# Kernel tuning notes

Hardware: AMD Instinct MI355X
Metric: run time of the kernel (lower is better)

## Reference

```python
import jax, jax.numpy as jnp
import numpy as np
from jax import lax

B, S, C, D, V = 256, 50, 40, 256, 20000
T_DIFF = 1000
BETA_START, BETA_END = 1e-4, 2e-2


def _lstm(x, Wih, Whh, bih, bhh):
    # x: [B,S,D]; single-layer LSTM, batch_first, eval mode (no dropout)
    Bb = x.shape[0]
    H = Whh.shape[1]
    def step(carry, xt):
        h, c = carry
        g = xt @ Wih.T + bih + h @ Whh.T + bhh  # [B,4H]
        i, f, gg, o = jnp.split(g, 4, axis=-1)
        i = jax.nn.sigmoid(i); f = jax.nn.sigmoid(f)
        gg = jnp.tanh(gg); o = jax.nn.sigmoid(o)
        c = f * c + i * gg
        h = o * jnp.tanh(c)
        return (h, c), h
    h0 = jnp.zeros((Bb, H), x.dtype)
    (_, _), hs = lax.scan(step, (h0, h0), x.transpose(1, 0, 2))
    return hs.transpose(1, 0, 2)  # [B,S,H]


def setup_inputs() -> dict:
    key = jax.random.key(0)
    ks = jax.random.split(key, 20)
    sc = 0.05
    inp = {
        'input_seqs': jax.random.randint(ks[0], (B, S, C), 0, V),
        'masks': jnp.zeros((B, S), jnp.int32),
        'lengths': jax.random.randint(ks[1], (B,), 1, S + 1),
        'seq_time_step': jax.random.uniform(ks[2], (B, S), jnp.float32),
        'code_masks': jnp.zeros((B, S, C), jnp.int32),
        'diffusion_time_t': jax.random.randint(ks[3], (B,), 0, T_DIFF),
        'normal_noise': jax.random.normal(ks[4], (B, S, D), jnp.float32),
        # learned parameters
        'emb': jax.random.normal(ks[5], (V + 1, D), jnp.float32) * sc,
        'Wih': jax.random.normal(ks[6], (4 * D, D), jnp.float32) * sc,
        'Whh': jax.random.normal(ks[7], (4 * D, D), jnp.float32) * sc,
        'bih': jnp.zeros((4 * D,), jnp.float32),
        'bhh': jnp.zeros((4 * D,), jnp.float32),
        'Whk': jax.random.normal(ks[8], (D, D), jnp.float32) * sc,
        'bhk': jnp.zeros((D,), jnp.float32),
        'W1': jax.random.normal(ks[9], (64, 2 * D), jnp.float32) * sc,
        'b1': jnp.zeros((64,), jnp.float32),
        'W2': jax.random.normal(ks[10], (2, 64), jnp.float32) * sc,
        'b2': jnp.zeros((2,), jnp.float32),
        'Wdiff': jax.random.normal(ks[11], (D, D), jnp.float32) * sc,
        'bdiff': jnp.zeros((D,), jnp.float32),
        'temb': jax.random.normal(ks[12], (T_DIFF, D), jnp.float32) * sc,
        'Wout': jax.random.normal(ks[13], (2, D), jnp.float32) * sc,
        'bout': jnp.zeros((2,), jnp.float32),
    }
    # padding_idx row zeroed like nn.Embedding(padding_idx=-1)
    inp['emb'] = inp['emb'].at[V].set(0.0)
    return inp


def reference(input_seqs, masks, lengths, seq_time_step, code_masks,
              diffusion_time_t, normal_noise,
              emb, Wih, Whh, bih, bhh, Whk, bhk, W1, b1, W2, b2,
              Wdiff, bdiff, temb, Wout, bout):
    # embedding sum over codes per visit
    x = emb[input_seqs].sum(axis=2)  # [B,S,D]
    rnn_out = _lstm(x, Wih, Whh, bih, bhh)  # [B,S,D]

    # vectorized alignment loop: e_k is ALWAYS x[:,0] (as in source),
    # position i>=1 attends between e_k and w_hk(rnn_out[i-1])
    w = rnn_out @ Whk.T + bhk  # [B,S,D]
    e_k = x[:, :1, :]  # [B,1,D]
    wprev = w[:, :-1, :]  # [B,S-1,D] -> timestep i uses w[i-1]
    cat = jnp.concatenate([jnp.broadcast_to(e_k, wprev.shape), wprev], -1)
    attn = jax.nn.softmax(jnp.tanh(cat @ W1.T + b1) @ W2.T + b2, axis=-1)  # [B,S-1,2]
    aligned_rest = e_k * attn[..., 0:1] + wprev * attn[..., 1:2]
    aligned_e_t = jnp.concatenate([e_k, aligned_rest], axis=1)  # [B,S,D]

    # diffusion noising (linear beta schedule as in ehr.yml defaults)
    betas = jnp.linspace(BETA_START, BETA_END, T_DIFF, dtype=jnp.float32)
    alpha = jnp.cumprod(1.0 - betas)[diffusion_time_t][:, None, None]
    noisy = aligned_e_t * jnp.sqrt(alpha) + normal_noise * jnp.sqrt(1.0 - alpha)

    # UNet surrogate (source unavailable): timestep-conditioned linear map
    predicted_noise = (noisy + temb[diffusion_time_t][:, None, :]) @ Wdiff + bdiff

    gen_x = aligned_e_t + (normal_noise - predicted_noise)
    pool_x = jnp.max(x, axis=1) @ Wout.T + bout  # [B,2]
    gen_pool_x = jnp.max(gen_x, axis=1) @ Wout.T + bout  # [B,2]
    return (pool_x, gen_pool_x, predicted_noise, normal_noise)
```

## Files before the change

### kernel.cpp

```cpp
#include <hip/hip_runtime.h>
#include <cmath>

#define Bb 256
#define Ss 50
#define Cc 40
#define Dd 256
#define Vv 20000

typedef __bf16 bf16;
typedef __bf16 bf16x8 __attribute__((ext_vector_type(8)));
typedef float f32x4 __attribute__((ext_vector_type(4)));
typedef unsigned long long u64;

#define GL2LDS(g, l) __builtin_amdgcn_global_load_lds( \
    (__attribute__((address_space(1))) void*)(g), \
    (__attribute__((address_space(3))) void*)(l), 16, 0, 0)

#define OFFB_GATES    0ull
#define OFFB_ALIGNED  0ull
#define OFFB_CAT      13107200ull
#define OFFB_TMPB     25952256ull
#define OFFB_H1       32505856ull
#define OFFB_ATTNW    35717120ull
#define OFFB_X        52428800ull
#define OFFB_XB       65536000ull
#define OFFB_RNNB     72089600ull
#define OFFB_W        78643200ull
#define OFFB_BAR      91750400ull
#define OFFB_WIHB     92012544ull
#define OFFB_WHHB     92536832ull
#define OFFB_WHKB     93061120ull
#define OFFB_W1B      93192192ull
#define OFFB_WDTB     93257728ull
#define OFFB_SALPHA   93388800ull
#define OFFB_SBETA    93389824ull

template<int BM, int BN, int ACT>
__global__ __launch_bounds__(256) void mfma_gemm(
    const bf16* __restrict__ A, int lda,
    const bf16* __restrict__ B, int ldb,
    const float* __restrict__ bias1, const float* __restrict__ bias2,
    float* __restrict__ C, int ldc, int K)
{
    constexpr int BK = 32;
    constexpr int NF = BN / 32;
    __shared__ bf16 As[BM * BK];
    __shared__ bf16 Bs[BN * BK];
    const int tid  = threadIdx.x;
    const int wave = tid >> 6;
    const int lane = tid & 63;
    const int m0 = blockIdx.x * BM;
    const int n0 = blockIdx.y * BN;
    const int wm = (wave >> 1) * 64;
    const int wn = (wave & 1) * (BN / 2);

    f32x4 acc[4][NF];
#pragma unroll
    for (int i = 0; i < 4; ++i)
#pragma unroll
        for (int j = 0; j < NF; ++j) acc[i][j] = (f32x4){0.f, 0.f, 0.f, 0.f};

    const int ar = tid >> 2;
    const int ac = tid & 3;
    const int sw = ac ^ (ar & 3);
    const int lr = lane & 15;
    const int q  = lane >> 4;

    for (int k0 = 0; k0 < K; k0 += BK) {
        __syncthreads();
#pragma unroll
        for (int it = 0; it < BM / 64; ++it) {
            const bf16* gp = A + (size_t)(m0 + it * 64 + ar) * lda + k0 + sw * 8;
            GL2LDS(gp, As + it * 2048 + wave * 512);
        }
#pragma unroll
        for (int it = 0; it < BN / 64; ++it) {
            const bf16* gp = B + (size_t)(n0 + it * 64 + ar) * ldb + k0 + sw * 8;
            GL2LDS(gp, Bs + it * 2048 + wave * 512);
        }
        __syncthreads();

        bf16x8 af[4], bfv[NF];
#pragma unroll
        for (int fm = 0; fm < 4; ++fm) {
            int m = wm + fm * 16 + lr;
            af[fm] = *(const bf16x8*)(As + m * 32 + ((q ^ (m & 3)) * 8));
        }
#pragma unroll
        for (int fn = 0; fn < NF; ++fn) {
            int n = wn + fn * 16 + lr;
            bfv[fn] = *(const bf16x8*)(Bs + n * 32 + ((q ^ (n & 3)) * 8));
        }
#pragma unroll
        for (int fm = 0; fm < 4; ++fm)
#pragma unroll
            for (int fn = 0; fn < NF; ++fn)
                acc[fm][fn] = __builtin_amdgcn_mfma_f32_16x16x32_bf16(
                    af[fm], bfv[fn], acc[fm][fn], 0, 0, 0);
    }

    const int rbase = q * 4;
#pragma unroll
    for (int fn = 0; fn < NF; ++fn) {
        const int col = n0 + wn + fn * 16 + lr;
        float bb = 0.f;
        if (bias1) bb += bias1[col];
        if (bias2) bb += bias2[col];
#pragma unroll
        for (int fm = 0; fm < 4; ++fm) {
            f32x4 v = acc[fm][fn];
#pragma unroll
            for (int r = 0; r < 4; ++r) {
                const int row = m0 + wm + fm * 16 + rbase + r;
                float val = v[r] + bb;
                if (ACT == 1) val = tanhf(val);
                C[(size_t)row * ldc + col] = val;
            }
        }
    }
}

__global__ __launch_bounds__(512, 2) void lstm_quad(
    const bf16* __restrict__ Whhb,
    const float* __restrict__ gates,
    bf16* __restrict__ rnnb,
    unsigned* __restrict__ bar)
{
    __shared__ bf16 hb0[16 * 256];
    __shared__ bf16 hb1[16 * 256];
    __shared__ float pacc[4][4][16][16];
    const int tid  = threadIdx.x;
    const int w    = tid >> 6;
    const int lane = tid & 63;
    const int lr   = lane & 15;
    const int q    = lane >> 4;
    const int bm   = blockIdx.x & 15;
    const int bd   = blockIdx.x >> 4;
    const int kh   = w >> 2;
    const int ct   = w & 3;
    const int dg   = bd * 64 + ct * 16 + lr;

    f32x4 wfr[4][4];
#pragma unroll
    for (int g = 0; g < 4; ++g) {
        const bf16* brow = Whhb + (size_t)(g * 256 + dg) * Dd + kh * 128 + q * 8;
#pragma unroll
        for (int kc = 0; kc < 4; ++kc)
            wfr[g][kc] = *(const f32x4*)(brow + kc * 32);
    }

    const float* gp[4];
#pragma unroll
    for (int r = 0; r < 4; ++r)
        gp[r] = gates + (size_t)(bm * 16 + q * 4 + r) * (Ss * 1024) + dg;

    const int xrow = tid >> 4, xc8 = tid & 15;
    const size_t my_base = ((size_t)(bm * 16 + xrow) * Ss) * Dd + bd * 64 + xc8 * 4;
    const int pack_off = xrow * 512 + (((bd * 8 + (xc8 >> 1)) ^ (xrow & 7)) << 4) + (xc8 & 1) * 8;

    const int pA  = tid >> 8;
    const int pdA = pA + (pA >= bd ? 1 : 0);
    const int pdB = 2 + (2 >= bd ? 1 : 0);
    const int rowA = (tid >> 4) & 15, xqA = tid & 15;
    const size_t gA = ((size_t)(bm * 16 + rowA) * Ss) * Dd + pdA * 64 + xqA * 4;
    const size_t gB = ((size_t)(bm * 16 + xrow) * Ss) * Dd + pdB * 64 + xc8 * 4;
    const int unpA = rowA * 512 + (((pdA * 8 + (xqA >> 1)) ^ (rowA & 7)) << 4) + (xqA & 1) * 8;
    const int unpB = xrow * 512 + (((pdB * 8 + (xc8 >> 1)) ^ (xrow & 7)) << 4) + (xc8 & 1) * 8;
    unsigned* myf = bar + (bm * 4 + bd) * 32;
    unsigned* pfA = bar + (bm * 4 + pdA) * 32;
    unsigned* pfB = bar + (bm * 4 + pdB) * 32;

    int ew_off[4];
#pragma unroll
    for (int r = 0; r < 4; ++r) {
        const int row = q * 4 + r;
        ew_off[r] = row * 512 + (((dg >> 3) ^ (row & 7)) << 4) + (dg & 7) * 2;
    }

    float c[4] = {0.f, 0.f, 0.f, 0.f};
    float gaA[4][4], gaB[4][4];
    if (kh == 0) {
#pragma unroll
        for (int r = 0; r < 4; ++r)
#pragma unroll
            for (int g = 0; g < 4; ++g) gaA[g][r] = gp[r][g * 256];
    }

#define STEP(T, GACUR, GANEXT, RD, WR, FIRST)                                   \
    {                                                                           \
        f32x4 acc[4];                                                           \
        _Pragma("unroll")                                                       \
        for (int g = 0; g < 4; ++g) acc[g] = (f32x4){0.f, 0.f, 0.f, 0.f};       \
        if (!(FIRST)) {                                                         \
            bf16x8 af[4];                                                       \
            _Pragma("unroll")                                                   \
            for (int kc = 0; kc < 4; ++kc)                                      \
                af[kc] = *(const bf16x8*)((const char*)(RD) + lr * 512          \
                         + (((kh * 16 + kc * 4 + q) ^ (lr & 7)) << 4));         \
            _Pragma("unroll")                                                   \
            for (int kc = 0; kc < 4; ++kc)                                      \
                _Pragma("unroll")                                               \
                for (int g = 0; g < 4; ++g)                                     \
                    acc[g] = __builtin_amdgcn_mfma_f32_16x16x32_bf16(           \
                        af[kc], __builtin_bit_cast(bf16x8, wfr[g][kc]),         \
                        acc[g], 0, 0, 0);                                       \
        }                                                                       \
        if (kh == 1) {                                                          \
            _Pragma("unroll")                                                   \
            for (int g = 0; g < 4; ++g)                                         \
                _Pragma("unroll")                                               \
                for (int r = 0; r < 4; ++r)                                     \
                    pacc[ct][g][q * 4 + r][lr] = acc[g][r];                     \
        }                                                                       \
        __syncthreads();                          \
        if (kh == 0) {                                                          \
            _Pragma("unroll")                                                   \
            for (int r = 0; r < 4; ++r) {                                       \
                float gi = acc[0][r] + pacc[ct][0][q * 4 + r][lr] + GACUR[0][r];\
                float gf = acc[1][r] + pacc[ct][1][q * 4 + r][lr] + GACUR[1][r];\
                float gg = acc[2][r] + pacc[ct][2][q * 4 + r][lr] + GACUR[2][r];\
                float go = acc[3][r] + pacc[ct][3][q * 4 + r][lr] + GACUR[3][r];\
                float ii  = 1.f / (1.f + expf(-gi));                            \
                float ff  = 1.f / (1.f + expf(-gf));                            \
                float g2t = tanhf(gg);                                          \
                float oo  = 1.f / (1.f + expf(-go));                            \
                c[r] = ff * c[r] + ii * g2t;                                    \
                *(bf16*)((char*)(WR) + ew_off[r]) = (bf16)(oo * tanhf(c[r]));   \
            }                                                                   \
        }                                                                       \
        __syncthreads();                          \
        if (tid < 256) {                                                        \
            u64 v = *(const u64*)((const char*)(WR) + pack_off);                \
            __hip_atomic_store((u64*)(rnnb + my_base + (size_t)(T) * Dd), v,    \
                               __ATOMIC_RELAXED, __HIP_MEMORY_SCOPE_AGENT);     \
        }                                                                       \
        if ((T) != Ss - 1) {                                                    \
            __syncthreads();        \
            if (tid == 0)                                                       \
                __hip_atomic_store(myf, (unsigned)((T) + 1),                    \
                                   __ATOMIC_RELAXED, __HIP_MEMORY_SCOPE_AGENT); \
            if (kh == 0) {            \
                _Pragma("unroll")                                               \
                for (int r = 0; r < 4; ++r)                                     \
                    _Pragma("unroll")                                           \
                    for (int g = 0; g < 4; ++g)                                 \
                        GANEXT[g][r] = gp[r][(size_t)((T) + 1) * 1024 + g * 256];\
            }                                                                   \
            while (__hip_atomic_load(pfA, __ATOMIC_RELAXED,                     \
                                     __HIP_MEMORY_SCOPE_AGENT)                  \
                   < (unsigned)((T) + 1)) {}                                    \
            {                                                                   \
                u64 rv = __hip_atomic_load(                                     \
                    (const u64*)(rnnb + gA + (size_t)(T) * Dd),                 \
                    __ATOMIC_RELAXED, __HIP_MEMORY_SCOPE_AGENT);                \
                *(u64*)((char*)(WR) + unpA) = rv;                               \
            }                                                                   \
            if (tid < 256) {                                                    \
                while (__hip_atomic_load(pfB, __ATOMIC_RELAXED,                 \
                                         __HIP_MEMORY_SCOPE_AGENT)              \
                       < (unsigned)((T) + 1)) {}                                \
                u64 rv = __hip_atomic_load(                                     \
                    (const u64*)(rnnb + gB + (size_t)(T) * Dd),                 \
                    __ATOMIC_RELAXED, __HIP_MEMORY_SCOPE_AGENT);                \
                *(u64*)((char*)(WR) + unpB) = rv;                               \
            }                                                                   \
            __syncthreads();           \
        }                                                                       \
    }

    for (int t2 = 0; t2 < Ss; t2 += 2) {
        STEP(t2,     gaA, gaB, hb1, hb0, (t2 == 0));
        STEP(t2 + 1, gaB, gaA, hb0, hb1, false);
    }
#undef STEP
}

__global__ __launch_bounds__(256) void prep_kernel(
    const float* __restrict__ Wih, bf16* __restrict__ Wihb,
    const float* __restrict__ Whh, bf16* __restrict__ Whhb,
    const float* __restrict__ Whk, bf16* __restrict__ Whkb,
    const float* __restrict__ W1,  bf16* __restrict__ W1b,
    const float* __restrict__ Wdiff, bf16* __restrict__ WdTb,
    const int* __restrict__ tdiff, float* __restrict__ salpha,
    float* __restrict__ sbeta, unsigned* __restrict__ bar)
{
    __shared__ float t[32][33];
    int bx = blockIdx.x;
    const int tid = threadIdx.x;
    if (bx < 1024) { int i = bx * 256 + tid; Wihb[i] = (bf16)Wih[i]; return; }
    bx -= 1024;
    if (bx < 1024) { int i = bx * 256 + tid; Whhb[i] = (bf16)Whh[i]; return; }
    bx -= 1024;
    if (bx < 256)  { int i = bx * 256 + tid; Whkb[i] = (bf16)Whk[i]; return; }
    bx -= 256;
    if (bx < 128)  { int i = bx * 256 + tid; W1b[i]  = (bf16)W1[i];  return; }
    bx -= 128;
    if (bx < 64) {
        const int c0 = (bx & 7) * 32, r0 = (bx >> 3) * 32;
        const int tx = tid & 31, ty = tid >> 5;
        for (int i = ty; i < 32; i += 8)
            t[i][tx] = Wdiff[(size_t)(r0 + i) * 256 + c0 + tx];
        __syncthreads();
        for (int i = ty; i < 32; i += 8)
            WdTb[(size_t)(c0 + i) * 256 + r0 + tx] = (bf16)t[tx][i];
        return;
    }
#pragma unroll
    for (int j = 0; j < 8; ++j) bar[tid * 8 + j] = 0u;
    const int tt = tdiff[tid];
    const float step = (0.02f - 1e-4f) / 999.f;
    float prod = 1.f;
    for (int j = 0; j <= tt; ++j) prod *= (1.f - (1e-4f + j * step));
    salpha[tid] = sqrtf(prod);
    sbeta[tid]  = sqrtf(fmaxf(1.f - prod, 0.f));
}

__global__ __launch_bounds__(256) void embed_kernel(
    const int* __restrict__ seqs, const float* __restrict__ emb,
    float* __restrict__ x, bf16* __restrict__ xb)
{
    __shared__ int idx[Cc];
    const int bs = blockIdx.x;
    const int tid = threadIdx.x;
    if (tid < Cc) idx[tid] = seqs[(size_t)bs * Cc + tid];
    __syncthreads();
    float s = 0.f;
#pragma unroll 8
    for (int c = 0; c < Cc; ++c) s += emb[(size_t)idx[c] * Dd + tid];
    x[(size_t)bs * Dd + tid]  = s;
    xb[(size_t)bs * Dd + tid] = (bf16)s;
}

__global__ __launch_bounds__(256) void cat_build_kernel(
    const float* __restrict__ x, const float* __restrict__ w, bf16* __restrict__ cat)
{
    const int r = blockIdx.x;
    const int b = r / (Ss - 1), t = r % (Ss - 1);
    const int d = threadIdx.x;
    cat[(size_t)r * 512 + d]       = (bf16)x[((size_t)b * Ss) * Dd + d];
    cat[(size_t)r * 512 + 256 + d] = (bf16)w[((size_t)b * Ss + t) * Dd + d];
}

__global__ __launch_bounds__(256) void attn2_kernel(
    const float* __restrict__ H1, const float* __restrict__ W2,
    const float* __restrict__ b2, float* __restrict__ attnw)
{
    const int r = blockIdx.x * 4 + (threadIdx.x >> 6);
    const int j = threadIdx.x & 63;
    float h = H1[(size_t)r * 64 + j];
    float v0 = h * W2[j];
    float v1 = h * W2[64 + j];
#pragma unroll
    for (int off = 32; off; off >>= 1) { v0 += __shfl_down(v0, off); v1 += __shfl_down(v1, off); }
    if (j == 0) {
        float z0 = v0 + b2[0], z1 = v1 + b2[1];
        float m = fmaxf(z0, z1);
        float e0 = expf(z0 - m), e1 = expf(z1 - m);
        float inv = 1.f / (e0 + e1);
        attnw[(size_t)r * 2 + 0] = e0 * inv;
        attnw[(size_t)r * 2 + 1] = e1 * inv;
    }
}

__global__ __launch_bounds__(256) void attn_diff_kernel(
    const float* __restrict__ x, const float* __restrict__ w,
    const float* __restrict__ attnw, const float* __restrict__ noise,
    const float* __restrict__ temb, const int* __restrict__ tdiff,
    const float* __restrict__ salpha, const float* __restrict__ sbeta,
    float* __restrict__ aligned, bf16* __restrict__ tmpb)
{
    const int bs = blockIdx.x;
    const int b = bs / Ss, s = bs % Ss;
    const int d = threadIdx.x;
    const float ek = x[((size_t)b * Ss) * Dd + d];
    float v;
    if (s == 0) {
        v = ek;
    } else {
        const int r = b * (Ss - 1) + (s - 1);
        const float a0 = attnw[(size_t)r * 2], a1 = attnw[(size_t)r * 2 + 1];
        v = ek * a0 + w[((size_t)b * Ss + s - 1) * Dd + d] * a1;
    }
    const size_t i = (size_t)bs * Dd + d;
    aligned[i] = v;
    const int t = tdiff[b];
    tmpb[i] = (bf16)(v * salpha[b] + noise[i] * sbeta[b] + temb[(size_t)t * Dd + d]);
}

__device__ inline void pool_reduce_write(float m, const float* __restrict__ Wout,
                                         const float* __restrict__ bout,
                                         float* __restrict__ outp, int b,
                                         float* r0, float* r1)
{
    float v0 = m * Wout[threadIdx.x];
    float v1 = m * Wout[Dd + threadIdx.x];
#pragma unroll
    for (int off = 32; off; off >>= 1) { v0 += __shfl_down(v0, off); v1 += __shfl_down(v1, off); }
    const int lane = threadIdx.x & 63, wv = threadIdx.x >> 6;
    if (lane == 0) { r0[wv] = v0; r1[wv] = v1; }
    __syncthreads();
    if (threadIdx.x == 0) {
        outp[b * 2 + 0] = r0[0] + r0[1] + r0[2] + r0[3] + bout[0];
        outp[b * 2 + 1] = r1[0] + r1[1] + r1[2] + r1[3] + bout[1];
    }
}

__global__ __launch_bounds__(256) void pool_x_kernel(
    const float* __restrict__ x, const float* __restrict__ Wout,
    const float* __restrict__ bout, float* __restrict__ outp)
{
    __shared__ float r0[4], r1[4];
    const int b = blockIdx.x, d = threadIdx.x;
    float m = -INFINITY;
    for (int s = 0; s < Ss; ++s) m = fmaxf(m, x[((size_t)b * Ss + s) * Dd + d]);
    pool_reduce_write(m, Wout, bout, outp, b, r0, r1);
}

__global__ __launch_bounds__(256) void gen_pool_kernel(
    const float* __restrict__ aligned, const float* __restrict__ noise,
    const float* __restrict__ pred, const float* __restrict__ Wout,
    const float* __restrict__ bout, float* __restrict__ outp)
{
    __shared__ float r0[4], r1[4];
    const int b = blockIdx.x, d = threadIdx.x;
    float m = -INFINITY;
    for (int s = 0; s < Ss; ++s) {
        const size_t i = ((size_t)b * Ss + s) * Dd + d;
        m = fmaxf(m, aligned[i] + noise[i] - pred[i]);
    }
    pool_reduce_write(m, Wout, bout, outp, b, r0, r1);
}

extern "C" void kernel_launch(void* const* d_in, const int* in_sizes, int n_in,
                              void* d_out, int out_size, void* d_ws, size_t ws_size,
                              hipStream_t stream)
{
    const int*   seqs  = (const int*)d_in[0];
    const int*   tdiff = (const int*)d_in[5];
    const float* noise = (const float*)d_in[6];
    const float* emb   = (const float*)d_in[7];
    const float* Wih   = (const float*)d_in[8];
    const float* Whh   = (const float*)d_in[9];
    const float* bih   = (const float*)d_in[10];
    const float* bhh   = (const float*)d_in[11];
    const float* Whk   = (const float*)d_in[12];
    const float* bhk   = (const float*)d_in[13];
    const float* W1    = (const float*)d_in[14];
    const float* b1    = (const float*)d_in[15];
    const float* W2    = (const float*)d_in[16];
    const float* b2    = (const float*)d_in[17];
    const float* Wdiff = (const float*)d_in[18];
    const float* bdiff = (const float*)d_in[19];
    const float* temb  = (const float*)d_in[20];
    const float* Wout  = (const float*)d_in[21];
    const float* bout  = (const float*)d_in[22];

    float* outp = (float*)d_out;
    char*  wsb  = (char*)d_ws;

    float* gates   = (float*)(wsb + OFFB_GATES);
    float* aligned = (float*)(wsb + OFFB_ALIGNED);
    bf16*  catb    = (bf16*) (wsb + OFFB_CAT);
    bf16*  tmpb    = (bf16*) (wsb + OFFB_TMPB);
    float* H1      = (float*)(wsb + OFFB_H1);
    float* attnw   = (float*)(wsb + OFFB_ATTNW);
    float* x       = (float*)(wsb + OFFB_X);
    bf16*  xb      = (bf16*) (wsb + OFFB_XB);
    bf16*  rnnb    = (bf16*) (wsb + OFFB_RNNB);
    float* wbuf    = (float*)(wsb + OFFB_W);
    unsigned* bar  = (unsigned*)(wsb + OFFB_BAR);
    bf16*  Wihb    = (bf16*) (wsb + OFFB_WIHB);
    bf16*  Whhb    = (bf16*) (wsb + OFFB_WHHB);
    bf16*  Whkb    = (bf16*) (wsb + OFFB_WHKB);
    bf16*  W1b     = (bf16*) (wsb + OFFB_W1B);
    bf16*  WdTb    = (bf16*) (wsb + OFFB_WDTB);
    float* salpha  = (float*)(wsb + OFFB_SALPHA);
    float* sbeta   = (float*)(wsb + OFFB_SBETA);

    float* pred_out  = outp + 1024;
    float* noise_out = outp + 1024 + (size_t)Bb * Ss * Dd;

    prep_kernel<<<2497, 256, 0, stream>>>(Wih, Wihb, Whh, Whhb, Whk, Whkb,
                                          W1, W1b, Wdiff, WdTb,
                                          tdiff, salpha, sbeta, bar);

    embed_kernel<<<Bb * Ss, 256, 0, stream>>>(seqs, emb, x, xb);

    pool_x_kernel<<<Bb, 256, 0, stream>>>(x, Wout, bout, outp);

    mfma_gemm<128, 128, 0><<<dim3(100, 8), 256, 0, stream>>>(
        xb, 256, Wihb, 256, bih, bhh, gates, 1024, 256);

    lstm_quad<<<64, 512, 0, stream>>>(Whhb, gates, rnnb, bar);

    mfma_gemm<128, 128, 0><<<dim3(100, 2), 256, 0, stream>>>(
        rnnb, 256, Whkb, 256, bhk, nullptr, wbuf, 256, 256);

    cat_build_kernel<<<Bb * (Ss - 1), 256, 0, stream>>>(x, wbuf, catb);
    mfma_gemm<128, 64, 1><<<dim3(98, 1), 256, 0, stream>>>(
        catb, 512, W1b, 512, b1, nullptr, H1, 64, 512);
    attn2_kernel<<<(Bb * (Ss - 1)) / 4, 256, 0, stream>>>(H1, W2, b2, attnw);

    attn_diff_kernel<<<Bb * Ss, 256, 0, stream>>>(
        x, wbuf, attnw, noise, temb, tdiff, salpha, sbeta, aligned, tmpb);

    mfma_gemm<128, 128, 0><<<dim3(100, 2), 256, 0, stream>>>(
        tmpb, 256, WdTb, 256, bdiff, nullptr, pred_out, 256, 256);

    gen_pool_kernel<<<Bb, 256, 0, stream>>>(aligned, noise, pred_out, Wout, bout, outp + 512);

    hipMemcpyAsync(noise_out, noise, (size_t)Bb * Ss * Dd * sizeof(float),
                   hipMemcpyDeviceToDevice, stream);
}
```

Baseline: 486.9 us.

## Replace LSTM cross-block flag barrier with tagged per-element hidden-state exchange

```diff
diff --git a/kernel.cpp b/kernel.cpp
--- a/kernel.cpp
+++ b/kernel.cpp
@@ -26,7 +26,7 @@
 #define OFFB_XB       65536000ull
 #define OFFB_RNNB     72089600ull
 #define OFFB_W        78643200ull
-#define OFFB_BAR      91750400ull
+#define OFFB_XCH0     91750400ull
 #define OFFB_WIHB     92012544ull
 #define OFFB_WHHB     92536832ull
 #define OFFB_WHKB     93061120ull
@@ -124,11 +124,12 @@
     const bf16* __restrict__ Whhb,
     const float* __restrict__ gates,
     bf16* __restrict__ rnnb,
-    unsigned* __restrict__ bar)
+    unsigned* __restrict__ xch0,
+    unsigned* __restrict__ xch1)
 {
     __shared__ bf16 hb0[16 * 256];
     __shared__ bf16 hb1[16 * 256];
-    __shared__ float pacc[4][4][16][16];
+    __shared__ float pacc[4][4][16][17];
     const int tid  = threadIdx.x;
     const int w    = tid >> 6;
     const int lane = tid & 63;
@@ -154,22 +155,12 @@
     for (int r = 0; r < 4; ++r)
         gp[r] = gates + (size_t)(bm * 16 + q * 4 + r) * (Ss * 1024) + dg;
 
+    const int myslot = (bm * 4 + bd) << 10;
+
     const int xrow = tid >> 4, xc8 = tid & 15;
     const size_t my_base = ((size_t)(bm * 16 + xrow) * Ss) * Dd + bd * 64 + xc8 * 4;
     const int pack_off = xrow * 512 + (((bd * 8 + (xc8 >> 1)) ^ (xrow & 7)) << 4) + (xc8 & 1) * 8;
 
-    const int pA  = tid >> 8;
-    const int pdA = pA + (pA >= bd ? 1 : 0);
-    const int pdB = 2 + (2 >= bd ? 1 : 0);
-    const int rowA = (tid >> 4) & 15, xqA = tid & 15;
-    const size_t gA = ((size_t)(bm * 16 + rowA) * Ss) * Dd + pdA * 64 + xqA * 4;
-    const size_t gB = ((size_t)(bm * 16 + xrow) * Ss) * Dd + pdB * 64 + xc8 * 4;
-    const int unpA = rowA * 512 + (((pdA * 8 + (xqA >> 1)) ^ (rowA & 7)) << 4) + (xqA & 1) * 8;
-    const int unpB = xrow * 512 + (((pdB * 8 + (xc8 >> 1)) ^ (xrow & 7)) << 4) + (xc8 & 1) * 8;
-    unsigned* myf = bar + (bm * 4 + bd) * 32;
-    unsigned* pfA = bar + (bm * 4 + pdA) * 32;
-    unsigned* pfB = bar + (bm * 4 + pdB) * 32;
-
     int ew_off[4];
 #pragma unroll
     for (int r = 0; r < 4; ++r) {
@@ -186,7 +177,7 @@
             for (int g = 0; g < 4; ++g) gaA[g][r] = gp[r][g * 256];
     }
 
-#define STEP(T, GACUR, GANEXT, RD, WR, FIRST)                                   \
+#define STEP(T, GACUR, GANEXT, RD, WR, XB, FIRST)                               \
     {                                                                           \
         f32x4 acc[4];                                                           \
         _Pragma("unroll")                                                       \
@@ -228,17 +219,27 @@
                 *(bf16*)((char*)(WR) + ew_off[r]) = (bf16)(oo * tanhf(c[r]));   \
             }                                                                   \
         }                                                                       \
-        __syncthreads();                          \
-        if (tid < 256) {                                                        \
+        __syncthreads();                        \
+        {               \
+            const unsigned tg = (unsigned)((T) + 1) << 16;                      \
+            _Pragma("unroll")                                                   \
+            for (int s = 0; s < 2; ++s) {                                       \
+                const int widx = tid * 2 + s;                                   \
+                const int row = widx >> 6, col = widx & 63;                     \
+                const int dgs = bd * 64 + col;                                  \
+                const int off = row * 512 + (((dgs >> 3) ^ (row & 7)) << 4)     \
+                                + (dgs & 7) * 2;                                \
+                unsigned short hv =                                             \
+                    *(const unsigned short*)((const char*)(WR) + off);          \
+                __hip_atomic_store((XB) + myslot + widx, tg | (unsigned)hv,     \
+                                   __ATOMIC_RELAXED, __HIP_MEMORY_SCOPE_AGENT); \
+            }                                                                   \
+        }                                                                       \
+        if (tid < 256) {           \
             u64 v = *(const u64*)((const char*)(WR) + pack_off);                \
-            __hip_atomic_store((u64*)(rnnb + my_base + (size_t)(T) * Dd), v,    \
-                               __ATOMIC_RELAXED, __HIP_MEMORY_SCOPE_AGENT);     \
+            *(u64*)(rnnb + my_base + (size_t)(T) * Dd) = v;                     \
         }                                                                       \
         if ((T) != Ss - 1) {                                                    \
-            __syncthreads();        \
-            if (tid == 0)                                                       \
-                __hip_atomic_store(myf, (unsigned)((T) + 1),                    \
-                                   __ATOMIC_RELAXED, __HIP_MEMORY_SCOPE_AGENT); \
             if (kh == 0) {            \
                 _Pragma("unroll")                                               \
                 for (int r = 0; r < 4; ++r)                                     \
@@ -246,31 +247,32 @@
                     for (int g = 0; g < 4; ++g)                                 \
                         GANEXT[g][r] = gp[r][(size_t)((T) + 1) * 1024 + g * 256];\
             }                                                                   \
-            while (__hip_atomic_load(pfA, __ATOMIC_RELAXED,                     \
-                                     __HIP_MEMORY_SCOPE_AGENT)                  \
-                   < (unsigned)((T) + 1)) {}                                    \
-            {                                                                   \
-                u64 rv = __hip_atomic_load(                                     \
-                    (const u64*)(rnnb + gA + (size_t)(T) * Dd),                 \
-                    __ATOMIC_RELAXED, __HIP_MEMORY_SCOPE_AGENT);                \
-                *(u64*)((char*)(WR) + unpA) = rv;                               \
+            {               \
+                const unsigned tv = (unsigned)((T) + 1);                        \
+                _Pragma("unroll")                                               \
+                for (int j = 0; j < 6; ++j) {                                   \
+                    const int rr = tid * 6 + j;                                 \
+                    const int p_ = rr >> 10, w2 = rr & 1023;                    \
+                    const int pd_ = p_ + (p_ >= bd ? 1 : 0);                    \
+                    const int row = w2 >> 6, col = w2 & 63;                     \
+                    const int dgp = pd_ * 64 + col;                             \
+                    unsigned v;                                                 \
+                    do {                                                        \
+                        v = __hip_atomic_load((XB) + ((bm * 4 + pd_) << 10) + w2,\
+                                __ATOMIC_RELAXED, __HIP_MEMORY_SCOPE_AGENT);    \
+                    } while ((v >> 16) != tv);                                  \
+                    const int off = row * 512 + (((dgp >> 3) ^ (row & 7)) << 4) \
+                                    + (dgp & 7) * 2;                            \
+                    *(unsigned short*)((char*)(WR) + off) = (unsigned short)v;  \
+                }                                                               \
             }                                                                   \
-            if (tid < 256) {                                                    \
-                while (__hip_atomic_load(pfB, __ATOMIC_RELAXED,                 \
-                                         __HIP_MEMORY_SCOPE_AGENT)              \
-                       < (unsigned)((T) + 1)) {}                                \
-                u64 rv = __hip_atomic_load(                                     \
-                    (const u64*)(rnnb + gB + (size_t)(T) * Dd),                 \
-                    __ATOMIC_RELAXED, __HIP_MEMORY_SCOPE_AGENT);                \
-                *(u64*)((char*)(WR) + unpB) = rv;                               \
-            }                                                                   \
-            __syncthreads();           \
+            __syncthreads();         \
         }                                                                       \
     }
 
     for (int t2 = 0; t2 < Ss; t2 += 2) {
-        STEP(t2,     gaA, gaB, hb1, hb0, (t2 == 0));
-        STEP(t2 + 1, gaB, gaA, hb0, hb1, false);
+        STEP(t2,     gaA, gaB, hb1, hb0, xch0, (t2 == 0));
+        STEP(t2 + 1, gaB, gaA, hb0, hb1, xch1, false);
     }
 #undef STEP
 }
@@ -282,7 +284,8 @@
     const float* __restrict__ W1,  bf16* __restrict__ W1b,
     const float* __restrict__ Wdiff, bf16* __restrict__ WdTb,
     const int* __restrict__ tdiff, float* __restrict__ salpha,
-    float* __restrict__ sbeta, unsigned* __restrict__ bar)
+    float* __restrict__ sbeta,
+    unsigned* __restrict__ xch0, unsigned* __restrict__ xch1)
 {
     __shared__ float t[32][33];
     int bx = blockIdx.x;
@@ -305,8 +308,10 @@
             WdTb[(size_t)(c0 + i) * 256 + r0 + tx] = (bf16)t[tx][i];
         return;
     }
-#pragma unroll
-    for (int j = 0; j < 8; ++j) bar[tid * 8 + j] = 0u;
+    bx -= 64;
+    if (bx < 256) { xch0[bx * 256 + tid] = 0u; return; }
+    bx -= 256;
+    if (bx < 256) { xch1[bx * 256 + tid] = 0u; return; }
     const int tt = tdiff[tid];
     const float step = (0.02f - 1e-4f) / 999.f;
     float prod = 1.f;
@@ -468,7 +473,8 @@
     bf16*  xb      = (bf16*) (wsb + OFFB_XB);
     bf16*  rnnb    = (bf16*) (wsb + OFFB_RNNB);
     float* wbuf    = (float*)(wsb + OFFB_W);
-    unsigned* bar  = (unsigned*)(wsb + OFFB_BAR);
+    unsigned* xch0 = (unsigned*)(wsb + OFFB_XCH0);
+    unsigned* xch1 = (unsigned*)(wsb + OFFB_W);
     bf16*  Wihb    = (bf16*) (wsb + OFFB_WIHB);
     bf16*  Whhb    = (bf16*) (wsb + OFFB_WHHB);
     bf16*  Whkb    = (bf16*) (wsb + OFFB_WHKB);
@@ -480,9 +486,9 @@
     float* pred_out  = outp + 1024;
     float* noise_out = outp + 1024 + (size_t)Bb * Ss * Dd;
 
-    prep_kernel<<<2497, 256, 0, stream>>>(Wih, Wihb, Whh, Whhb, Whk, Whkb,
+    prep_kernel<<<3009, 256, 0, stream>>>(Wih, Wihb, Whh, Whhb, Whk, Whkb,
                                           W1, W1b, Wdiff, WdTb,
-                                          tdiff, salpha, sbeta, bar);
+                                          tdiff, salpha, sbeta, xch0, xch1);
 
     embed_kernel<<<Bb * Ss, 256, 0, stream>>>(seqs, emb, x, xb);
 
@@ -491,7 +497,7 @@
     mfma_gemm<128, 128, 0><<<dim3(100, 8), 256, 0, stream>>>(
         xb, 256, Wihb, 256, bih, bhh, gates, 1024, 256);
 
-    lstm_quad<<<64, 512, 0, stream>>>(Whhb, gates, rnnb, bar);
+    lstm_quad<<<64, 512, 0, stream>>>(Whhb, gates, rnnb, xch0, xch1);
 
     mfma_gemm<128, 128, 0><<<dim3(100, 2), 256, 0, stream>>>(
         rnnb, 256, Whkb, 256, bhk, nullptr, wbuf, 256, 256);
```

After: 503.8 us. 1.03x slower.

## Fuse attention concat into H1 GEMM and attn2 into diffusion kernel

Applied to the files above, without the earlier changes.

```diff
diff --git a/kernel.cpp b/kernel.cpp
--- a/kernel.cpp
+++ b/kernel.cpp
@@ -18,10 +18,9 @@
 
 #define OFFB_GATES    0ull
 #define OFFB_ALIGNED  0ull
-#define OFFB_CAT      13107200ull
+#define OFFB_WBB      13107200ull
 #define OFFB_TMPB     25952256ull
 #define OFFB_H1       32505856ull
-#define OFFB_ATTNW    35717120ull
 #define OFFB_X        52428800ull
 #define OFFB_XB       65536000ull
 #define OFFB_RNNB     72089600ull
@@ -40,7 +39,7 @@
     const bf16* __restrict__ A, int lda,
     const bf16* __restrict__ B, int ldb,
     const float* __restrict__ bias1, const float* __restrict__ bias2,
-    float* __restrict__ C, int ldc, int K)
+    float* __restrict__ C, bf16* __restrict__ Cb, int ldc, int K)
 {
     constexpr int BK = 32;
     constexpr int NF = BN / 32;
@@ -115,6 +114,89 @@
                 float val = v[r] + bb;
                 if (ACT == 1) val = tanhf(val);
                 C[(size_t)row * ldc + col] = val;
+                if (Cb) Cb[(size_t)row * ldc + col] = (bf16)val;
+            }
+        }
+    }
+}
+
+__global__ __launch_bounds__(256) void h1_gemm(
+    const bf16* __restrict__ xb, const bf16* __restrict__ wbb,
+    const bf16* __restrict__ W1b,
+    const float* __restrict__ b1, float* __restrict__ H1)
+{
+    constexpr int BM = 128, BN = 64, BK = 32, NF = 2;
+    constexpr int K = 512;
+    __shared__ bf16 As[BM * BK];
+    __shared__ bf16 Bs[BN * BK];
+    const int tid  = threadIdx.x;
+    const int wave = tid >> 6;
+    const int lane = tid & 63;
+    const int m0 = blockIdx.x * BM;
+    const int wm = (wave >> 1) * 64;
+    const int wn = (wave & 1) * 32;
+
+    f32x4 acc[4][NF];
+#pragma unroll
+    for (int i = 0; i < 4; ++i)
+#pragma unroll
+        for (int j = 0; j < NF; ++j) acc[i][j] = (f32x4){0.f, 0.f, 0.f, 0.f};
+
+    const int ar = tid >> 2;
+    const int ac = tid & 3;
+    const int sw = ac ^ (ar & 3);
+    const int lr = lane & 15;
+    const int q  = lane >> 4;
+
+    for (int k0 = 0; k0 < K; k0 += BK) {
+        __syncthreads();
+#pragma unroll
+        for (int it = 0; it < 2; ++it) {
+            const int row = m0 + it * 64 + ar;
+            const int b = row / (Ss - 1), t = row - b * (Ss - 1);
+            const int col = k0 + sw * 8;
+            const bf16* gp = (col < 256)
+                ? xb  + (size_t)b * (Ss * Dd) + col
+                : wbb + ((size_t)(b * Ss + t)) * Dd + (col - 256);
+            GL2LDS(gp, As + it * 2048 + wave * 512);
+        }
+        {
+            const bf16* gp = W1b + (size_t)ar * K + k0 + sw * 8;
+            GL2LDS(gp, Bs + wave * 512);
+        }
+        __syncthreads();
+
+        bf16x8 af[4], bfv[NF];
+#pragma unroll
+        for (int fm = 0; fm < 4; ++fm) {
+            int m = wm + fm * 16 + lr;
+            af[fm] = *(const bf16x8*)(As + m * 32 + ((q ^ (m & 3)) * 8));
+        }
+#pragma unroll
+        for (int fn = 0; fn < NF; ++fn) {
+            int n = wn + fn * 16 + lr;
+            bfv[fn] = *(const bf16x8*)(Bs + n * 32 + ((q ^ (n & 3)) * 8));
+        }
+#pragma unroll
+        for (int fm = 0; fm < 4; ++fm)
+#pragma unroll
+            for (int fn = 0; fn < NF; ++fn)
+                acc[fm][fn] = __builtin_amdgcn_mfma_f32_16x16x32_bf16(
+                    af[fm], bfv[fn], acc[fm][fn], 0, 0, 0);
+    }
+
+    const int rbase = q * 4;
+#pragma unroll
+    for (int fn = 0; fn < NF; ++fn) {
+        const int col = wn + fn * 16 + lr;
+        const float bb = b1[col];
+#pragma unroll
+        for (int fm = 0; fm < 4; ++fm) {
+            f32x4 v = acc[fm][fn];
+#pragma unroll
+            for (int r = 0; r < 4; ++r) {
+                const int row = m0 + wm + fm * 16 + rbase + r;
+                H1[(size_t)row * 64 + col] = tanhf(v[r] + bb);
             }
         }
     }
@@ -128,7 +210,7 @@
 {
     __shared__ bf16 hb0[16 * 256];
     __shared__ bf16 hb1[16 * 256];
-    __shared__ float pacc[4][4][16][16];
+    __shared__ float pacc[4][4][16][17];
     const int tid  = threadIdx.x;
     const int w    = tid >> 6;
     const int lane = tid & 63;
@@ -331,60 +413,49 @@
     xb[(size_t)bs * Dd + tid] = (bf16)s;
 }
 
-__global__ __launch_bounds__(256) void cat_build_kernel(
-    const float* __restrict__ x, const float* __restrict__ w, bf16* __restrict__ cat)
-{
-    const int r = blockIdx.x;
-    const int b = r / (Ss - 1), t = r % (Ss - 1);
-    const int d = threadIdx.x;
-    cat[(size_t)r * 512 + d]       = (bf16)x[((size_t)b * Ss) * Dd + d];
-    cat[(size_t)r * 512 + 256 + d] = (bf16)w[((size_t)b * Ss + t) * Dd + d];
-}
-
-__global__ __launch_bounds__(256) void attn2_kernel(
-    const float* __restrict__ H1, const float* __restrict__ W2,
-    const float* __restrict__ b2, float* __restrict__ attnw)
-{
-    const int r = blockIdx.x * 4 + (threadIdx.x >> 6);
-    const int j = threadIdx.x & 63;
-    float h = H1[(size_t)r * 64 + j];
-    float v0 = h * W2[j];
-    float v1 = h * W2[64 + j];
-#pragma unroll
-    for (int off = 32; off; off >>= 1) { v0 += __shfl_down(v0, off); v1 += __shfl_down(v1, off); }
-    if (j == 0) {
-        float z0 = v0 + b2[0], z1 = v1 + b2[1];
-        float m = fmaxf(z0, z1);
-        float e0 = expf(z0 - m), e1 = expf(z1 - m);
-        float inv = 1.f / (e0 + e1);
-        attnw[(size_t)r * 2 + 0] = e0 * inv;
-        attnw[(size_t)r * 2 + 1] = e1 * inv;
-    }
-}
-
 __global__ __launch_bounds__(256) void attn_diff_kernel(
     const float* __restrict__ x, const float* __restrict__ w,
-    const float* __restrict__ attnw, const float* __restrict__ noise,
+    const float* __restrict__ H1, const float* __restrict__ W2,
+    const float* __restrict__ b2, const float* __restrict__ noise,
     const float* __restrict__ temb, const int* __restrict__ tdiff,
     const float* __restrict__ salpha, const float* __restrict__ sbeta,
-    float* __restrict__ aligned, bf16* __restrict__ tmpb)
-{
+    float* __restrict__ aligned, bf16* __restrict__ tmpb,
+    float* __restrict__ noise_out)
+{
+    __shared__ float sa[2];
     const int bs = blockIdx.x;
     const int b = bs / Ss, s = bs % Ss;
     const int d = threadIdx.x;
+    if (s > 0 && threadIdx.x < 64) {
+        const int r = b * (Ss - 1) + (s - 1);
+        const int j = threadIdx.x;
+        float h = H1[(size_t)r * 64 + j];
+        float v0 = h * W2[j];
+        float v1 = h * W2[64 + j];
+#pragma unroll
+        for (int off = 32; off; off >>= 1) { v0 += __shfl_down(v0, off); v1 += __shfl_down(v1, off); }
+        if (j == 0) {
+            float z0 = v0 + b2[0], z1 = v1 + b2[1];
+            float m = fmaxf(z0, z1);
+            float e0 = expf(z0 - m), e1 = expf(z1 - m);
+            float inv = 1.f / (e0 + e1);
+            sa[0] = e0 * inv;
+            sa[1] = e1 * inv;
+        }
+    }
+    __syncthreads();
     const float ek = x[((size_t)b * Ss) * Dd + d];
     float v;
     if (s == 0) {
         v = ek;
     } else {
-        const int r = b * (Ss - 1) + (s - 1);
-        const float a0 = attnw[(size_t)r * 2], a1 = attnw[(size_t)r * 2 + 1];
-        v = ek * a0 + w[((size_t)b * Ss + s - 1) * Dd + d] * a1;
+        v = ek * sa[0] + w[((size_t)b * Ss + s - 1) * Dd + d] * sa[1];
     }
     const size_t i = (size_t)bs * Dd + d;
     aligned[i] = v;
     const int t = tdiff[b];
     tmpb[i] = (bf16)(v * salpha[b] + noise[i] * sbeta[b] + temb[(size_t)t * Dd + d]);
+    noise_out[i] = noise[i];
 }
 
 __device__ inline void pool_reduce_write(float m, const float* __restrict__ Wout,
@@ -460,10 +531,9 @@
 
     float* gates   = (float*)(wsb + OFFB_GATES);
     float* aligned = (float*)(wsb + OFFB_ALIGNED);
-    bf16*  catb    = (bf16*) (wsb + OFFB_CAT);
+    bf16*  wbb     = (bf16*) (wsb + OFFB_WBB);
     bf16*  tmpb    = (bf16*) (wsb + OFFB_TMPB);
     float* H1      = (float*)(wsb + OFFB_H1);
-    float* attnw   = (float*)(wsb + OFFB_ATTNW);
     float* x       = (float*)(wsb + OFFB_X);
     bf16*  xb      = (bf16*) (wsb + OFFB_XB);
     bf16*  rnnb    = (bf16*) (wsb + OFFB_RNNB);
@@ -489,26 +559,21 @@
     pool_x_kernel<<<Bb, 256, 0, stream>>>(x, Wout, bout, outp);
 
     mfma_gemm<128, 128, 0><<<dim3(100, 8), 256, 0, stream>>>(
-        xb, 256, Wihb, 256, bih, bhh, gates, 1024, 256);
+        xb, 256, Wihb, 256, bih, bhh, gates, nullptr, 1024, 256);
 
     lstm_quad<<<64, 512, 0, stream>>>(Whhb, gates, rnnb, bar);
 
     mfma_gemm<128, 128, 0><<<dim3(100, 2), 256, 0, stream>>>(
-        rnnb, 256, Whkb, 256, bhk, nullptr, wbuf, 256, 256);
-
-    cat_build_kernel<<<Bb * (Ss - 1), 256, 0, stream>>>(x, wbuf, catb);
-    mfma_gemm<128, 64, 1><<<dim3(98, 1), 256, 0, stream>>>(
-        catb, 512, W1b, 512, b1, nullptr, H1, 64, 512);
-    attn2_kernel<<<(Bb * (Ss - 1)) / 4, 256, 0, stream>>>(H1, W2, b2, attnw);
+        rnnb, 256, Whkb, 256, bhk, nullptr, wbuf, wbb, 256, 256);
+
+    h1_gemm<<<dim3(98, 1), 256, 0, stream>>>(xb, wbb, W1b, b1, H1);
 
     attn_diff_kernel<<<Bb * Ss, 256, 0, stream>>>(
-        x, wbuf, attnw, noise, temb, tdiff, salpha, sbeta, aligned, tmpb);
+        x, wbuf, H1, W2, b2, noise, temb, tdiff, salpha, sbeta,
+        aligned, tmpb, noise_out);
 
     mfma_gemm<128, 128, 0><<<dim3(100, 2), 256, 0, stream>>>(
-        tmpb, 256, WdTb, 256, bdiff, nullptr, pred_out, 256, 256);
+        tmpb, 256, WdTb, 256, bdiff, nullptr, pred_out, nullptr, 256, 256);
 
     gen_pool_kernel<<<Bb, 256, 0, stream>>>(aligned, noise, pred_out, Wout, bout, outp + 512);
-
-    hipMemcpyAsync(noise_out, noise, (size_t)Bb * Ss * Dd * sizeof(float),
-                   hipMemcpyDeviceToDevice, stream);
-}
+}
```

After: 480.4 us. Within noise of the previous version (-1.3%).
